# Optimization experiments

Measured on AMD Instinct MI355X. Metric: run time of the kernel, lower is better.

The kernel has to match this reference:

```python
import jax, jax.numpy as jnp
import numpy as np

NUM_USERS = 100000
NUM_ITEMS = 50000
NUM_EDGES = 1000000
H = 64            # initial embedding dim
DIMS = [64, 64]   # per-layer output dims
B = 16384         # BPR batch size
NEG_SLOPE = 0.2
EPS = 1e-12


def setup_inputs() -> dict:
    key = jax.random.key(0)
    ks = jax.random.split(key, 20)
    s = 1.0 / np.sqrt(H)
    inp = {
        'user_emb': jax.random.normal(ks[0], (NUM_USERS, H), jnp.float32) * 0.1,
        'item_emb': jax.random.normal(ks[1], (NUM_ITEMS, H), jnp.float32) * 0.1,
        'W1_0': jax.random.normal(ks[2], (H, DIMS[0]), jnp.float32) * s,
        'b1_0': jnp.zeros((DIMS[0],), jnp.float32),
        'W2_0': jax.random.normal(ks[3], (H, DIMS[0]), jnp.float32) * s,
        'b2_0': jnp.zeros((DIMS[0],), jnp.float32),
        'W1_1': jax.random.normal(ks[4], (DIMS[0], DIMS[1]), jnp.float32) * s,
        'b1_1': jnp.zeros((DIMS[1],), jnp.float32),
        'W2_1': jax.random.normal(ks[5], (DIMS[0], DIMS[1]), jnp.float32) * s,
        'b2_1': jnp.zeros((DIMS[1],), jnp.float32),
        'edge_index': jnp.stack([
            jax.random.randint(ks[6], (NUM_EDGES,), 0, NUM_USERS),
            jax.random.randint(ks[7], (NUM_EDGES,), 0, NUM_ITEMS),
        ], axis=0),
        'users': jax.random.randint(ks[8], (B,), 0, NUM_USERS),
        'pos_items': jax.random.randint(ks[9], (B,), 0, NUM_ITEMS),
        'neg_items': jax.random.randint(ks[10], (B,), 0, NUM_ITEMS),
    }
    return inp


def _edge_norm(src, dst):
    # symmetric sqrt-degree norm: (deg_src * deg_dst) ** -0.5 per edge
    ones = jnp.ones(src.shape[0], jnp.float32)
    du = jax.ops.segment_sum(ones, src, num_segments=NUM_USERS)[src]
    di = jax.ops.segment_sum(ones, dst, num_segments=NUM_ITEMS)[dst]
    return ((du * di) ** -0.5)[:, None]  # [E, 1]


def _epilogue(h):
    # leaky_relu(0.2) -> (dropout eval = identity) -> L2 row-normalize
    h = jnp.where(h >= 0, h, NEG_SLOPE * h)
    n = jnp.sqrt(jnp.sum(h * h, axis=1, keepdims=True))
    return h / jnp.maximum(n, EPS)


def _layer(u, i, src, dst, norm, W1, b1, W2, b2):
    # node-level W1 transform, gathered per edge (same math as per-edge W1(x_j))
    u1 = u @ W1 + b1            # [Nu, d]
    i1 = i @ W1 + b1            # [Ni, d]
    cross = u[src] * i[dst]     # [E, din]  shared by both directions
    mW2 = cross @ W2 + b2       # [E, d]
    # user -> item: x_j = user[src], aggregate at item dst
    out_i = jax.ops.segment_sum(norm * u1[src] + mW2, dst, num_segments=NUM_ITEMS)
    # item -> user: x_j = item[dst], aggregate at user src
    out_u = jax.ops.segment_sum(norm * i1[dst] + mW2, src, num_segments=NUM_USERS)
    return _epilogue(out_u), _epilogue(out_i)


def reference(user_emb, item_emb, W1_0, b1_0, W2_0, b2_0, W1_1, b1_1, W2_1, b2_1,
              edge_index, users, pos_items, neg_items):
    src, dst = edge_index[0], edge_index[1]
    norm = _edge_norm(src, dst)
    u_list, i_list = [user_emb], [item_emb]
    u, i = user_emb, item_emb
    u, i = _layer(u, i, src, dst, norm, W1_0, b1_0, W2_0, b2_0)
    u_list.append(u); i_list.append(i)
    u, i = _layer(u, i, src, dst, norm, W1_1, b1_1, W2_1, b2_1)
    u_list.append(u); i_list.append(i)
    user_all = jnp.concatenate(u_list, axis=1)   # [Nu, H+sum(DIMS)]
    item_all = jnp.concatenate(i_list, axis=1)   # [Ni, H+sum(DIMS)]
    return (user_all[users], item_all[pos_items], item_all[neg_items])
```

## Files before the change

kernel.cpp:

```cpp
#include <hip/hip_runtime.h>

#define NU 100000
#define NI 50000
#define NE 1000000
#define NB 16384

#define UB ((NU + 1023) / 1024)
#define IB ((NI + 1023) / 1024)

__global__ void deg_kernel(const int* __restrict__ ei, int* du, int* di) {
    int e = blockIdx.x * blockDim.x + threadIdx.x;
    if (e >= NE) return;
    atomicAdd(&du[ei[e]], 1);
    atomicAdd(&di[ei[NE + e]], 1);
}

__global__ __launch_bounds__(1024) void scan1_kernel(
        const int* __restrict__ du, const int* __restrict__ di,
        int* __restrict__ psum, float* __restrict__ rsd_u, float* __restrict__ rsd_i) {
    int b = blockIdx.x, tid = threadIdx.x;
    int v = 0;
    if (b < UB) {
        int i = b * 1024 + tid;
        if (i < NU) {
            int d = du[i]; v = d;
            rsd_u[i] = d > 0 ? 1.0f / sqrtf((float)d) : 0.f;
        }
    } else {
        int i = (b - UB) * 1024 + tid;
        if (i < NI) {
            int d = di[i]; v = d;
            rsd_i[i] = d > 0 ? 1.0f / sqrtf((float)d) : 0.f;
        }
    }
    int s = v;
    #pragma unroll
    for (int off = 32; off > 0; off >>= 1) s += __shfl_xor(s, off);
    __shared__ int ws[16];
    if ((tid & 63) == 0) ws[tid >> 6] = s;
    __syncthreads();
    if (tid == 0) {
        int t = 0;
        #pragma unroll
        for (int w = 0; w < 16; ++w) t += ws[w];
        psum[b] = t;
    }
}

__global__ __launch_bounds__(128) void scan2_kernel(int* __restrict__ psum) {
    int base = (blockIdx.x == 0) ? 0 : UB;
    int n = (blockIdx.x == 0) ? UB : IB;
    int tid = threadIdx.x;
    __shared__ int sh[128];
    int v = (tid < n) ? psum[base + tid] : 0;
    sh[tid] = v;
    __syncthreads();
    for (int off = 1; off < 128; off <<= 1) {
        int t = (tid >= off) ? sh[tid - off] : 0;
        __syncthreads();
        sh[tid] += t;
        __syncthreads();
    }
    if (tid < n) psum[base + tid] = sh[tid] - v;
}

__global__ __launch_bounds__(1024) void scan3_kernel(
        const int* __restrict__ du, const int* __restrict__ di,
        const int* __restrict__ psum,
        int* __restrict__ rp_u, int* __restrict__ rp_i,
        int* __restrict__ cur_u, int* __restrict__ cur_i) {
    int b = blockIdx.x, tid = threadIdx.x;
    const int* deg; int* rp; int* cur; int N; int i0;
    if (b < UB) { deg = du; rp = rp_u; cur = cur_u; N = NU; i0 = b * 1024; }
    else        { deg = di; rp = rp_i; cur = cur_i; N = NI; i0 = (b - UB) * 1024; }
    int i = i0 + tid;
    int v = (i < N) ? deg[i] : 0;
    __shared__ int sh[1024];
    sh[tid] = v;
    __syncthreads();
    for (int off = 1; off < 1024; off <<= 1) {
        int t = (tid >= off) ? sh[tid - off] : 0;
        __syncthreads();
        sh[tid] += t;
        __syncthreads();
    }
    int excl = sh[tid] - v + psum[b];
    if (i < N) { rp[i] = excl; cur[i] = excl; }
    if (b == 0 && tid == 0) { rp_u[NU] = NE; rp_i[NI] = NE; }
}

__global__ void fill_csr_kernel(const int* __restrict__ ei,
                                int* __restrict__ curu, int* __restrict__ curi,
                                int* __restrict__ csr_u, int* __restrict__ csr_i) {
    int e = blockIdx.x * blockDim.x + threadIdx.x;
    if (e >= NE) return;
    int s = ei[e], d = ei[NE + e];
    int si = atomicAdd(&curi[d], 1);
    csr_i[si] = s;
    int su = atomicAdd(&curu[s], 1);
    csr_u[su] = d;
}

#define BATCH 4
__global__ __launch_bounds__(512) void gt_fused_kernel(
        const float* __restrict__ xu, const float* __restrict__ xi,
        const int* __restrict__ rpu, const int* __restrict__ rpi,
        const int* __restrict__ csru, const int* __restrict__ csri,
        const float* __restrict__ rsdu, const float* __restrict__ rsdi,
        const float* __restrict__ W1, const float* __restrict__ b1,
        const float* __restrict__ W2, const float* __restrict__ b2,
        float* __restrict__ outu, float* __restrict__ outi) {
    __shared__ float w1s[64 * 64];
    __shared__ float w2s[64 * 64];
    __shared__ float acs[8][BATCH][128];
    int tid = threadIdx.x;
    #pragma unroll
    for (int r = 0; r < 8; ++r) {
        w1s[r * 512 + tid] = W1[r * 512 + tid];
        w2s[r * 512 + tid] = W2[r * 512 + tid];
    }
    __syncthreads();
    int wv = tid >> 6, lane = tid & 63;
    float b1v = b1[lane], b2v = b2[lane];
    const int NG = (NI + NU + 31) / 32;
    for (int g = blockIdx.x; g < NG; g += gridDim.x) {
        int nbase = g * 32 + wv * BATCH;
        float ba[BATCH], dg[BATCH];
        #pragma unroll
        for (int j = 0; j < BATCH; ++j) {
            int n = nbase + j;
            bool act = n < NI + NU;
            bool isItem = n < NI;
            int nn = isItem ? n : n - NI;
            const int* rp     = isItem ? rpi : rpu;
            const int* cs     = isItem ? csri : csru;
            const float* xin  = isItem ? xi : xu;
            const float* embo = isItem ? xu : xi;
            const float* rso  = isItem ? rsdu : rsdi;
            const float* rown = isItem ? rsdi : rsdu;
            float sp = 0.f, ss = 0.f, sw = 0.f, rs = 0.f, dgf = 0.f, xv = 0.f;
            if (act) {
                int beg = rp[nn], end = rp[nn + 1];
                dgf = (float)(end - beg);
                rs = rown[nn];
                xv = xin[nn * 64 + lane];
                int jj = beg;
                for (; jj + 3 < end; jj += 4) {
                    int i0 = cs[jj], i1 = cs[jj + 1], i2 = cs[jj + 2], i3 = cs[jj + 3];
                    float w0 = rso[i0], w1v = rso[i1], w2v = rso[i2], w3v = rso[i3];
                    float v0 = embo[i0 * 64 + lane];
                    float v1 = embo[i1 * 64 + lane];
                    float v2 = embo[i2 * 64 + lane];
                    float v3 = embo[i3 * 64 + lane];
                    sp += (v0 + v1) + (v2 + v3);
                    ss += w0 * v0 + w1v * v1 + w2v * v2 + w3v * v3;
                    sw += (w0 + w1v) + (w2v + w3v);
                }
                for (; jj < end; ++jj) {
                    int i0 = cs[jj];
                    float w0 = rso[i0];
                    float v0 = embo[i0 * 64 + lane];
                    sp += v0; ss += w0 * v0; sw += w0;
                }
            }
            ba[j] = rs * sw;
            dg[j] = dgf;
            acs[wv][j][lane] = rs * ss;
            acs[wv][j][64 + lane] = xv * sp;
        }
        float acc[BATCH] = {0.f, 0.f, 0.f, 0.f};
        #pragma unroll 4
        for (int kq = 0; kq < 16; ++kq) {
            float4 av[BATCH], cv[BATCH];
            #pragma unroll
            for (int j = 0; j < BATCH; ++j) {
                av[j] = *(const float4*)&acs[wv][j][kq * 4];
                cv[j] = *(const float4*)&acs[wv][j][64 + kq * 4];
            }
            #pragma unroll
            for (int kk = 0; kk < 4; ++kk) {
                int k = kq * 4 + kk;
                float w1v = w1s[k * 64 + lane];
                float w2v = w2s[k * 64 + lane];
                #pragma unroll
                for (int j = 0; j < BATCH; ++j) {
                    float a = (&av[j].x)[kk], c = (&cv[j].x)[kk];
                    acc[j] += a * w1v + c * w2v;
                }
            }
        }
        #pragma unroll
        for (int j = 0; j < BATCH; ++j) {
            int n = nbase + j;
            if (n >= NI + NU) continue;
            bool isItem = n < NI;
            int nn = isItem ? n : n - NI;
            float* outp = isItem ? outi : outu;
            float h = acc[j] + ba[j] * b1v + dg[j] * b2v;
            h = h >= 0.f ? h : 0.2f * h;
            float nsq = h * h;
            #pragma unroll
            for (int off = 32; off > 0; off >>= 1) nsq += __shfl_xor(nsq, off);
            float nrm = sqrtf(nsq);
            outp[nn * 64 + lane] = h / fmaxf(nrm, 1e-12f);
        }
    }
}

__global__ void gather_kernel(const float* __restrict__ ue, const float* __restrict__ u1,
                              const float* __restrict__ u2, const float* __restrict__ ie,
                              const float* __restrict__ i1, const float* __restrict__ i2,
                              const int* __restrict__ users, const int* __restrict__ pos,
                              const int* __restrict__ neg, float4* __restrict__ out) {
    int idx = blockIdx.x * blockDim.x + threadIdx.x;
    if (idx >= 3 * NB * 48) return;
    int which = idx / (NB * 48);
    int rem = idx - which * (NB * 48);
    int b = rem / 48, c4 = rem - b * 48;
    int seg = c4 >> 4, cc = (c4 & 15) << 2;
    int row;
    const float* srcarr;
    if (which == 0) {
        row = users[b];
        srcarr = (seg == 0) ? ue : (seg == 1 ? u1 : u2);
    } else {
        row = (which == 1) ? pos[b] : neg[b];
        srcarr = (seg == 0) ? ie : (seg == 1 ? i1 : i2);
    }
    out[idx] = *(const float4*)&srcarr[(size_t)row * 64 + cc];
}

extern "C" void kernel_launch(void* const* d_in, const int* in_sizes, int n_in,
                              void* d_out, int out_size, void* d_ws, size_t ws_size,
                              hipStream_t stream) {
    const float* user_emb = (const float*)d_in[0];
    const float* item_emb = (const float*)d_in[1];
    const float* W1_0 = (const float*)d_in[2];
    const float* b1_0 = (const float*)d_in[3];
    const float* W2_0 = (const float*)d_in[4];
    const float* b2_0 = (const float*)d_in[5];
    const float* W1_1 = (const float*)d_in[6];
    const float* b1_1 = (const float*)d_in[7];
    const float* W2_1 = (const float*)d_in[8];
    const float* b2_1 = (const float*)d_in[9];
    const int* ei = (const int*)d_in[10];
    const int* users = (const int*)d_in[11];
    const int* pos = (const int*)d_in[12];
    const int* neg = (const int*)d_in[13];

    char* p = (char*)d_ws;
    int* du = (int*)p;        p += NU * 4;
    int* di = (int*)p;        p += NI * 4;
    float* rsd_u = (float*)p; p += NU * 4;
    float* rsd_i = (float*)p; p += NI * 4;
    int* psum = (int*)p;      p += (UB + IB) * 4;
    int* rp_u = (int*)p;      p += (NU + 1) * 4;
    int* rp_i = (int*)p;      p += (NI + 1) * 4;
    int* cur_u = (int*)p;     p += NU * 4;
    int* cur_i = (int*)p;     p += NI * 4;
    int* csr_u = (int*)p;     p += (size_t)NE * 4;
    int* csr_i = (int*)p;     p += (size_t)NE * 4;
    float* u1 = (float*)p;    p += (size_t)NU * 64 * 4;
    float* u2 = (float*)p;    p += (size_t)NU * 64 * 4;
    float* i1 = (float*)p;    p += (size_t)NI * 64 * 4;
    float* i2 = (float*)p;    p += (size_t)NI * 64 * 4;

    hipMemsetAsync(du, 0, (size_t)(NU + NI) * sizeof(int), stream);

    deg_kernel<<<(NE + 255) / 256, 256, 0, stream>>>(ei, du, di);
    scan1_kernel<<<UB + IB, 1024, 0, stream>>>(du, di, psum, rsd_u, rsd_i);
    scan2_kernel<<<2, 128, 0, stream>>>(psum);
    scan3_kernel<<<UB + IB, 1024, 0, stream>>>(du, di, psum, rp_u, rp_i, cur_u, cur_i);
    fill_csr_kernel<<<(NE + 255) / 256, 256, 0, stream>>>(ei, cur_u, cur_i, csr_u, csr_i);

    gt_fused_kernel<<<2048, 512, 0, stream>>>(user_emb, item_emb, rp_u, rp_i, csr_u, csr_i,
                                              rsd_u, rsd_i, W1_0, b1_0, W2_0, b2_0, u1, i1);
    gt_fused_kernel<<<2048, 512, 0, stream>>>(u1, i1, rp_u, rp_i, csr_u, csr_i,
                                              rsd_u, rsd_i, W1_1, b1_1, W2_1, b2_1, u2, i2);

    gather_kernel<<<(3 * NB * 48 + 255) / 256, 256, 0, stream>>>(
        user_emb, u1, u2, item_emb, i1, i2, users, pos, neg, (float4*)d_out);
}
```

Measured before the change: 787.6 us.

## Split fused layer kernel into neighbor-gather and dense-transform kernels

Replaces the single fused gather-plus-matmul kernel with two kernels per node type: one wave per node gathers neighbor embeddings, loading the neighbor indices cooperatively and broadcasting them with shuffles, then writes 128-float aggregates to a global buffer. A second kernel applies the W1/W2 transform with bias, leaky ReLU and L2 normalization over 8 nodes per wave. The goal is to decouple the latency-bound irregular gather from the compute phase and to raise occupancy, since the gather kernel no longer holds 32 KB of weights in shared memory. The cost is an extra global round trip for the intermediate buffer and four times as many kernel launches per layer.

```diff
diff --git a/kernel.cpp b/kernel.cpp
--- a/kernel.cpp
+++ b/kernel.cpp
@@ -101,109 +101,100 @@
     csr_u[su] = d;
 }
 
-#define BATCH 4
-__global__ __launch_bounds__(512) void gt_fused_kernel(
-        const float* __restrict__ xu, const float* __restrict__ xi,
-        const int* __restrict__ rpu, const int* __restrict__ rpi,
-        const int* __restrict__ csru, const int* __restrict__ csri,
-        const float* __restrict__ rsdu, const float* __restrict__ rsdi,
+__global__ __launch_bounds__(256) void gatherA_kernel(
+        int N, const float* __restrict__ x_own, const float* __restrict__ emb_o,
+        const int* __restrict__ rp, const int* __restrict__ cs,
+        const float* __restrict__ rsd_own, const float* __restrict__ rsd_o,
+        float* __restrict__ acbuf, float* __restrict__ swbuf) {
+    int wv = (blockIdx.x * blockDim.x + threadIdx.x) >> 6;
+    int lane = threadIdx.x & 63;
+    if (wv >= N) return;
+    int beg = rp[wv], end = rp[wv + 1];
+    float sp = 0.f, ss = 0.f, swp = 0.f;
+    for (int jj = beg; jj < end; jj += 64) {
+        int m = min(64, end - jj);
+        int idx = (lane < m) ? cs[jj + lane] : 0;
+        float w = (lane < m) ? rsd_o[idx] : 0.f;
+        swp += w;
+        int t = 0;
+        for (; t + 3 < m; t += 4) {
+            int s0 = __shfl(idx, t),     s1 = __shfl(idx, t + 1);
+            int s2 = __shfl(idx, t + 2), s3 = __shfl(idx, t + 3);
+            float w0 = __shfl(w, t),     w1 = __shfl(w, t + 1);
+            float w2 = __shfl(w, t + 2), w3 = __shfl(w, t + 3);
+            float v0 = emb_o[(size_t)s0 * 64 + lane];
+            float v1 = emb_o[(size_t)s1 * 64 + lane];
+            float v2 = emb_o[(size_t)s2 * 64 + lane];
+            float v3 = emb_o[(size_t)s3 * 64 + lane];
+            sp += (v0 + v1) + (v2 + v3);
+            ss += w0 * v0 + w1 * v1 + w2 * v2 + w3 * v3;
+        }
+        for (; t < m; ++t) {
+            int s0 = __shfl(idx, t);
+            float w0 = __shfl(w, t);
+            float v0 = emb_o[(size_t)s0 * 64 + lane];
+            sp += v0; ss += w0 * v0;
+        }
+    }
+    #pragma unroll
+    for (int off = 32; off > 0; off >>= 1) swp += __shfl_xor(swp, off);
+    float rs = rsd_own[wv];
+    acbuf[(size_t)wv * 128 + lane] = rs * ss;
+    acbuf[(size_t)wv * 128 + 64 + lane] = x_own[(size_t)wv * 64 + lane] * sp;
+    if (lane == 0) swbuf[wv] = rs * swp;
+}
+
+#define TB 8
+__global__ __launch_bounds__(256) void transformB_kernel(
+        int N, const float* __restrict__ acbuf, const float* __restrict__ swbuf,
+        const int* __restrict__ rp,
         const float* __restrict__ W1, const float* __restrict__ b1,
         const float* __restrict__ W2, const float* __restrict__ b2,
-        float* __restrict__ outu, float* __restrict__ outi) {
-    __shared__ float w1s[64 * 64];
-    __shared__ float w2s[64 * 64];
-    __shared__ float acs[8][BATCH][128];
+        float* __restrict__ out) {
+    __shared__ float w1s[4096];
+    __shared__ float w2s[4096];
     int tid = threadIdx.x;
     #pragma unroll
-    for (int r = 0; r < 8; ++r) {
-        w1s[r * 512 + tid] = W1[r * 512 + tid];
-        w2s[r * 512 + tid] = W2[r * 512 + tid];
+    for (int r = 0; r < 4; ++r) {
+        *(float4*)&w1s[(r * 256 + tid) * 4] = *(const float4*)&W1[(r * 256 + tid) * 4];
+        *(float4*)&w2s[(r * 256 + tid) * 4] = *(const float4*)&W2[(r * 256 + tid) * 4];
     }
     __syncthreads();
     int wv = tid >> 6, lane = tid & 63;
+    int n0 = (blockIdx.x * 4 + wv) * TB;
+    if (n0 >= N) return;
     float b1v = b1[lane], b2v = b2[lane];
-    const int NG = (NI + NU + 31) / 32;
-    for (int g = blockIdx.x; g < NG; g += gridDim.x) {
-        int nbase = g * 32 + wv * BATCH;
-        float ba[BATCH], dg[BATCH];
-        #pragma unroll
-        for (int j = 0; j < BATCH; ++j) {
-            int n = nbase + j;
-            bool act = n < NI + NU;
-            bool isItem = n < NI;
-            int nn = isItem ? n : n - NI;
-            const int* rp     = isItem ? rpi : rpu;
-            const int* cs     = isItem ? csri : csru;
-            const float* xin  = isItem ? xi : xu;
-            const float* embo = isItem ? xu : xi;
-            const float* rso  = isItem ? rsdu : rsdi;
-            const float* rown = isItem ? rsdi : rsdu;
-            float sp = 0.f, ss = 0.f, sw = 0.f, rs = 0.f, dgf = 0.f, xv = 0.f;
-            if (act) {
-                int beg = rp[nn], end = rp[nn + 1];
-                dgf = (float)(end - beg);
-                rs = rown[nn];
-                xv = xin[nn * 64 + lane];
-                int jj = beg;
-                for (; jj + 3 < end; jj += 4) {
-                    int i0 = cs[jj], i1 = cs[jj + 1], i2 = cs[jj + 2], i3 = cs[jj + 3];
-                    float w0 = rso[i0], w1v = rso[i1], w2v = rso[i2], w3v = rso[i3];
-                    float v0 = embo[i0 * 64 + lane];
-                    float v1 = embo[i1 * 64 + lane];
-                    float v2 = embo[i2 * 64 + lane];
-                    float v3 = embo[i3 * 64 + lane];
-                    sp += (v0 + v1) + (v2 + v3);
-                    ss += w0 * v0 + w1v * v1 + w2v * v2 + w3v * v3;
-                    sw += (w0 + w1v) + (w2v + w3v);
-                }
-                for (; jj < end; ++jj) {
-                    int i0 = cs[jj];
-                    float w0 = rso[i0];
-                    float v0 = embo[i0 * 64 + lane];
-                    sp += v0; ss += w0 * v0; sw += w0;
-                }
-            }
-            ba[j] = rs * sw;
-            dg[j] = dgf;
-            acs[wv][j][lane] = rs * ss;
-            acs[wv][j][64 + lane] = xv * sp;
-        }
-        float acc[BATCH] = {0.f, 0.f, 0.f, 0.f};
-        #pragma unroll 4
-        for (int kq = 0; kq < 16; ++kq) {
-            float4 av[BATCH], cv[BATCH];
+    float acc[TB] = {0.f, 0.f, 0.f, 0.f, 0.f, 0.f, 0.f, 0.f};
+    for (int kq = 0; kq < 16; ++kq) {
+        float4 aq[TB], cq[TB];
+        #pragma unroll
+        for (int j = 0; j < TB; ++j) {
+            int n = n0 + j; if (n >= N) n = N - 1;
+            aq[j] = *(const float4*)&acbuf[(size_t)n * 128 + kq * 4];
+            cq[j] = *(const float4*)&acbuf[(size_t)n * 128 + 64 + kq * 4];
+        }
+        #pragma unroll
+        for (int kk = 0; kk < 4; ++kk) {
+            int k = kq * 4 + kk;
+            float w1v = w1s[k * 64 + lane];
+            float w2v = w2s[k * 64 + lane];
             #pragma unroll
-            for (int j = 0; j < BATCH; ++j) {
-                av[j] = *(const float4*)&acs[wv][j][kq * 4];
-                cv[j] = *(const float4*)&acs[wv][j][64 + kq * 4];
-            }
-            #pragma unroll
-            for (int kk = 0; kk < 4; ++kk) {
-                int k = kq * 4 + kk;
-                float w1v = w1s[k * 64 + lane];
-                float w2v = w2s[k * 64 + lane];
-                #pragma unroll
-                for (int j = 0; j < BATCH; ++j) {
-                    float a = (&av[j].x)[kk], c = (&cv[j].x)[kk];
-                    acc[j] += a * w1v + c * w2v;
-                }
-            }
-        }
-        #pragma unroll
-        for (int j = 0; j < BATCH; ++j) {
-            int n = nbase + j;
-            if (n >= NI + NU) continue;
-            bool isItem = n < NI;
-            int nn = isItem ? n : n - NI;
-            float* outp = isItem ? outi : outu;
-            float h = acc[j] + ba[j] * b1v + dg[j] * b2v;
-            h = h >= 0.f ? h : 0.2f * h;
-            float nsq = h * h;
-            #pragma unroll
-            for (int off = 32; off > 0; off >>= 1) nsq += __shfl_xor(nsq, off);
-            float nrm = sqrtf(nsq);
-            outp[nn * 64 + lane] = h / fmaxf(nrm, 1e-12f);
-        }
+            for (int j = 0; j < TB; ++j)
+                acc[j] += (&aq[j].x)[kk] * w1v + (&cq[j].x)[kk] * w2v;
+        }
+    }
+    #pragma unroll
+    for (int j = 0; j < TB; ++j) {
+        int n = n0 + j;
+        if (n >= N) break;
+        float dgf = (float)(rp[n + 1] - rp[n]);
+        float h = acc[j] + swbuf[n] * b1v + dgf * b2v;
+        h = h >= 0.f ? h : 0.2f * h;
+        float nsq = h * h;
+        #pragma unroll
+        for (int off = 32; off > 0; off >>= 1) nsq += __shfl_xor(nsq, off);
+        float nrm = sqrtf(nsq);
+        out[(size_t)n * 64 + lane] = h / fmaxf(nrm, 1e-12f);
     }
 }
 
@@ -264,6 +255,8 @@
     float* u2 = (float*)p;    p += (size_t)NU * 64 * 4;
     float* i1 = (float*)p;    p += (size_t)NI * 64 * 4;
     float* i2 = (float*)p;    p += (size_t)NI * 64 * 4;
+    float* acbuf = (float*)p; p += (size_t)NU * 128 * 4;
+    float* swbuf = (float*)p; p += NU * 4;
 
     hipMemsetAsync(du, 0, (size_t)(NU + NI) * sizeof(int), stream);
 
@@ -273,10 +266,28 @@
     scan3_kernel<<<UB + IB, 1024, 0, stream>>>(du, di, psum, rp_u, rp_i, cur_u, cur_i);
     fill_csr_kernel<<<(NE + 255) / 256, 256, 0, stream>>>(ei, cur_u, cur_i, csr_u, csr_i);
 
-    gt_fused_kernel<<<2048, 512, 0, stream>>>(user_emb, item_emb, rp_u, rp_i, csr_u, csr_i,
-                                              rsd_u, rsd_i, W1_0, b1_0, W2_0, b2_0, u1, i1);
-    gt_fused_kernel<<<2048, 512, 0, stream>>>(u1, i1, rp_u, rp_i, csr_u, csr_i,
-                                              rsd_u, rsd_i, W1_1, b1_1, W2_1, b2_1, u2, i2);
+    const int GA_I = (NI * 64 + 255) / 256;
+    const int GA_U = (NU * 64 + 255) / 256;
+    const int GB_I = (NI + 31) / 32;
+    const int GB_U = (NU + 31) / 32;
+
+    gatherA_kernel<<<GA_I, 256, 0, stream>>>(NI, item_emb, user_emb, rp_i, csr_i,
+                                             rsd_i, rsd_u, acbuf, swbuf);
+    transformB_kernel<<<GB_I, 256, 0, stream>>>(NI, acbuf, swbuf, rp_i,
+                                                W1_0, b1_0, W2_0, b2_0, i1);
+    gatherA_kernel<<<GA_U, 256, 0, stream>>>(NU, user_emb, item_emb, rp_u, csr_u,
+                                             rsd_u, rsd_i, acbuf, swbuf);
+    transformB_kernel<<<GB_U, 256, 0, stream>>>(NU, acbuf, swbuf, rp_u,
+                                                W1_0, b1_0, W2_0, b2_0, u1);
+
+    gatherA_kernel<<<GA_I, 256, 0, stream>>>(NI, i1, u1, rp_i, csr_i,
+                                             rsd_i, rsd_u, acbuf, swbuf);
+    transformB_kernel<<<GB_I, 256, 0, stream>>>(NI, acbuf, swbuf, rp_i,
+                                                W1_1, b1_1, W2_1, b2_1, i2);
+    gatherA_kernel<<<GA_U, 256, 0, stream>>>(NU, u1, i1, rp_u, csr_u,
+                                             rsd_u, rsd_i, acbuf, swbuf);
+    transformB_kernel<<<GB_U, 256, 0, stream>>>(NU, acbuf, swbuf, rp_u,
+                                                W1_1, b1_1, W2_1, b2_1, u2);
 
     gather_kernel<<<(3 * NB * 48 + 255) / 256, 256, 0, stream>>>(
         user_emb, u1, u2, item_emb, i1, i2, users, pos, neg, (float4*)d_out);
```

New measurement: 918.0 us. 1.17x slower.
